# Performance work log

Measured on AMD Instinct MI355X. Metric: run time of the kernel, lower is better.

## Reference

```python
import jax, jax.numpy as jnp
import numpy as np

NF, NA, NC = 100000, 400, 30   # flight, airport, carrier node counts
N = NF + NA + NC               # total nodes after type concatenation
D = 256                        # hidden_channels
B = 3                          # num_bases
R = 4                          # num_relations
E = 250000                     # edges per relation


def setup_inputs() -> dict:
    key = jax.random.key(0)
    ks = jax.random.split(key, 32)
    inp = {
        'x_flight': jax.random.normal(ks[0], (NF, 32), jnp.float32),
        'x_airport': jax.random.normal(ks[1], (NA, 16), jnp.float32),
        'x_carrier': jax.random.normal(ks[2], (NC, 8), jnp.float32),
        # per-type encoders (Linear stored as [in, out])
        'W_f': jax.random.normal(ks[3], (32, D), jnp.float32) * 0.05,
        'b_f': jnp.zeros((D,), jnp.float32),
        'W_a': jax.random.normal(ks[4], (16, D), jnp.float32) * 0.05,
        'b_a': jnp.zeros((D,), jnp.float32),
        'W_c': jax.random.normal(ks[5], (8, D), jnp.float32) * 0.05,
        'b_c': jnp.zeros((D,), jnp.float32),
        # RGCNConv layer 0: basis decomposition W_r = sum_b comp[r,b] * basis[b]
        'basis0': jax.random.normal(ks[6], (B, D, D), jnp.float32) * 0.02,
        'comp0': jax.random.normal(ks[7], (R, B), jnp.float32) * 0.5,
        'root0': jax.random.normal(ks[8], (D, D), jnp.float32) * 0.02,
        'bias0': jnp.zeros((D,), jnp.float32),
        # RGCNConv layer 1
        'basis1': jax.random.normal(ks[9], (B, D, D), jnp.float32) * 0.02,
        'comp1': jax.random.normal(ks[10], (R, B), jnp.float32) * 0.5,
        'root1': jax.random.normal(ks[11], (D, D), jnp.float32) * 0.02,
        'bias1': jnp.zeros((D,), jnp.float32),
        # readout Linear(D -> 1)
        'W_out': jax.random.normal(ks[12], (D, 1), jnp.float32) * 0.05,
        'b_out': jnp.zeros((1,), jnp.float32),
        # per-relation edge lists (local indices within src/dst node type)
        'src0': jax.random.randint(ks[13], (E,), 0, NF),
        'dst0': jax.random.randint(ks[14], (E,), 0, NA),
        'src1': jax.random.randint(ks[15], (E,), 0, NA),
        'dst1': jax.random.randint(ks[16], (E,), 0, NF),
        'src2': jax.random.randint(ks[17], (E,), 0, NF),
        'dst2': jax.random.randint(ks[18], (E,), 0, NC),
        'src3': jax.random.randint(ks[19], (E,), 0, NC),
        'dst3': jax.random.randint(ks[20], (E,), 0, NF),
    }
    return inp


def _rgcn_conv(x, basis, comp, root, bias, edges):
    """PyG RGCNConv with basis decomposition, mean aggregation per relation."""
    W = jnp.einsum('rb,bio->rio', comp, basis)  # [R, D, D]
    out = x @ root + bias                        # root/self transform
    for r, (src, dst) in enumerate(edges):       # R=4 fixed relations
        msg = x[src] @ W[r]                                        # [E, D]
        agg = jax.ops.segment_sum(msg, dst, num_segments=N)        # [N, D]
        deg = jax.ops.segment_sum(jnp.ones((dst.shape[0],), x.dtype), dst,
                                  num_segments=N)
        out = out + agg / jnp.maximum(deg, 1.0)[:, None]           # mean aggr
    return out


def reference(x_flight, x_airport, x_carrier,
              W_f, b_f, W_a, b_a, W_c, b_c,
              basis0, comp0, root0, bias0,
              basis1, comp1, root1, bias1,
              W_out, b_out,
              src0, dst0, src1, dst1, src2, dst2, src3, dst3):
    # per-type encoders + ReLU, then concat into homogeneous node tensor
    hf = jax.nn.relu(x_flight @ W_f + b_f)
    ha = jax.nn.relu(x_airport @ W_a + b_a)
    hc = jax.nn.relu(x_carrier @ W_c + b_c)
    x = jnp.concatenate([hf, ha, hc], axis=0)  # offsets: flight=0, airport=NF, carrier=NF+NA
    edges = [
        (src0, dst0 + NF),        # flight -> airport
        (src1 + NF, dst1),        # airport -> flight
        (src2, dst2 + NF + NA),   # flight -> carrier
        (src3 + NF + NA, dst3),   # carrier -> flight
    ]
    x = jax.nn.relu(_rgcn_conv(x, basis0, comp0, root0, bias0, edges))
    x = jax.nn.relu(_rgcn_conv(x, basis1, comp1, root1, bias1, edges))
    # dropout is identity in eval mode
    return (x[:NF] @ W_out + b_out).squeeze(-1)  # [NF]
```

## Files before the change

### kernel.cpp

```cpp
#include <hip/hip_runtime.h>
#include <hip/hip_bf16.h>
#include <cstdint>
#include <cstddef>

constexpr int NF = 100000;
constexpr int NA = 400;
constexpr int NC = 30;
constexpr int NN = NF + NA + NC;
constexpr int D  = 256;
constexpr int DD = D * D;
constexpr int E  = 250000;
constexpr int NSL = 128;
constexpr int FBLK = (NF + 127) / 128;
constexpr int TAILB = (NA + NC + 7) / 8;
constexpr int F13B = (2 * E + 511) / 512;
constexpr int AGGB = NA * 4 + NC * 64;
constexpr int YB   = (NA + NC) / 2;

constexpr int K1_HIST_END = 2 * NSL;
constexpr int K1_DEG_END  = K1_HIST_END + (2 * E + 255) / 256;
constexpr int K1_WS0_END  = K1_DEG_END + 256;
constexpr int K1_WS1_END  = K1_WS0_END + 256;
constexpr int K1_WR0_END  = K1_WS1_END + 1024;
constexpr int K1_WR1_END  = K1_WR0_END + 1024;

constexpr int W_ENC_END  = FBLK;
constexpr int W_TAIL_END = W_ENC_END + TAILB;
constexpr int W_F13_END  = W_TAIL_END + F13B;
constexpr int W_TOTAL    = W_F13_END + 2 * NSL;

typedef __attribute__((ext_vector_type(8))) short bf16x8;
typedef __attribute__((ext_vector_type(4))) float f32x4;
typedef __attribute__((ext_vector_type(8))) ushort u16x8;

__device__ inline ushort f2bf(float f) {
    __hip_bfloat16 h = __float2bfloat16(f);
    return __builtin_bit_cast(ushort, h);
}
__device__ inline float bf2f(ushort u) {
    __hip_bfloat16 h = __builtin_bit_cast(__hip_bfloat16, u);
    return __bfloat162float(h);
}

__device__ inline void gload_lds16(const ushort* g, ushort* l) {
    __builtin_amdgcn_global_load_lds(
        (const __attribute__((address_space(1))) void*)g,
        (__attribute__((address_space(3))) void*)l, 16, 0, 0);
}

__global__ __launch_bounds__(256) void prep_kernel(
    const int* __restrict__ dst0, const int* __restrict__ dst2,
    int* __restrict__ bh0, int* __restrict__ bh2,
    float* __restrict__ aggz,
    const float* __restrict__ Wf, ushort* __restrict__ WfTH, ushort* __restrict__ WfTL,
    const int* __restrict__ dst1, const int* __restrict__ dst3,
    int* __restrict__ deg1, int* __restrict__ deg3,
    const float* __restrict__ root0, ushort* __restrict__ WtH0, ushort* __restrict__ WtL0,
    const float* __restrict__ root1, ushort* __restrict__ WtH1, ushort* __restrict__ WtL1,
    const float* __restrict__ basis0, const float* __restrict__ comp0, float* __restrict__ wr0,
    const float* __restrict__ basis1, const float* __restrict__ comp1, float* __restrict__ wr1)
{
    __shared__ int hist[NA];
    const int b = blockIdx.x;
    const int t = threadIdx.x;
    if (b < K1_HIST_END) {
        for (int i = b * 256 + t; i < (NA + NC) * D; i += K1_HIST_END * 256)
            aggz[i] = 0.f;
        if (b < 32) {
            float wv = Wf[(size_t)b * D + t];
            ushort hi = f2bf(wv);
            WfTH[(size_t)t * 32 + b] = hi;
            WfTL[(size_t)t * 32 + b] = f2bf(wv - bf2f(hi));
        }
        bool isR2 = (b >= NSL);
        int sl = isR2 ? b - NSL : b;
        const int* dst = isR2 ? dst2 : dst0;
        int nb = isR2 ? NC : NA;
        for (int i = t; i < nb; i += 256) hist[i] = 0;
        __syncthreads();
        int lo = (int)((long long)E * sl / NSL);
        int hi = (int)((long long)E * (sl + 1) / NSL);
        for (int e = lo + t; e < hi; e += 256)
            atomicAdd(&hist[dst[e]], 1);
        __syncthreads();
        int* bh = isR2 ? (bh2 + sl * NC) : (bh0 + sl * NA);
        for (int i = t; i < nb; i += 256) bh[i] = hist[i];
    } else if (b < K1_DEG_END) {
        int idx = (b - K1_HIST_END) * 256 + t;
        if (idx < 2 * E) {
            if (idx < E) atomicAdd(&deg1[dst1[idx]], 1);
            else         atomicAdd(&deg3[dst3[idx - E]], 1);
        }
    } else if (b < K1_WS0_END) {
        int n = b - K1_DEG_END;
        float w = root0[(size_t)t * D + n];
        ushort hi = f2bf(w);
        WtH0[(size_t)n * D + t] = hi;
        WtL0[(size_t)n * D + t] = f2bf(w - bf2f(hi));
    } else if (b < K1_WS1_END) {
        int n = b - K1_WS0_END;
        float w = root1[(size_t)t * D + n];
        ushort hi = f2bf(w);
        WtH1[(size_t)n * D + t] = hi;
        WtL1[(size_t)n * D + t] = f2bf(w - bf2f(hi));
    } else if (b < K1_WR0_END) {
        int idx = (b - K1_WS1_END) * 256 + t;
        int r = idx >> 16;
        int io = idx & (DD - 1);
        wr0[idx] = comp0[r * 3 + 0] * basis0[io]
                 + comp0[r * 3 + 1] * basis0[DD + io]
                 + comp0[r * 3 + 2] * basis0[2 * DD + io];
    } else {
        int idx = (b - K1_WR0_END) * 256 + t;
        int r = idx >> 16;
        int io = idx & (DD - 1);
        wr1[idx] = comp1[r * 3 + 0] * basis1[io]
                 + comp1[r * 3 + 1] * basis1[DD + io]
                 + comp1[r * 3 + 2] * basis1[2 * DD + io];
    }
}

__global__ __launch_bounds__(1024) void scan_kernel(
    const int* __restrict__ deg1, const int* __restrict__ deg3,
    int* __restrict__ bsum,
    int* __restrict__ bh0, int* __restrict__ bh2,
    int* __restrict__ rp0, int* __restrict__ rp2,
    float* __restrict__ inv0, float* __restrict__ inv2)
{
    __shared__ int s[1024];
    __shared__ int tot[512];
    __shared__ int exc[512];
    const int b = blockIdx.x;
    const int t = threadIdx.x;
    if (b < 196) {
        bool isR3 = (b >= 98);
        const int* deg = isR3 ? deg3 : deg1;
        int chunk = isR3 ? b - 98 : b;
        int i = chunk * 1024 + t;
        int v = (i < NF) ? deg[i] : 0;
        s[t] = v;
        __syncthreads();
        for (int ofs = 512; ofs > 0; ofs >>= 1) {
            if (t < ofs) s[t] += s[t + ofs];
            __syncthreads();
        }
        if (t == 0) bsum[(isR3 ? 128 : 0) + chunk] = s[0];
        return;
    }
    int cnt = 0;
    if (t < NA) {
        int ss = 0;
        for (int sl = 0; sl < NSL; ++sl) {
            int v = bh0[sl * NA + t]; bh0[sl * NA + t] = ss; ss += v;
        }
        cnt = ss;
    } else if (t < NA + NC) {
        int bin = t - NA; int ss = 0;
        for (int sl = 0; sl < NSL; ++sl) {
            int v = bh2[sl * NC + bin]; bh2[sl * NC + bin] = ss; ss += v;
        }
        cnt = ss;
    }
    if (t < 512) tot[t] = cnt;
    __syncthreads();
    for (int ofs = 1; ofs < 512; ofs <<= 1) {
        int v = 0;
        if (t < 512 && t >= ofs) v = tot[t - ofs];
        __syncthreads();
        if (t < 512) tot[t] += v;
        __syncthreads();
    }
    if (t < 512) {
        int ex = tot[t] - cnt;
        if (t < NA) {
            exc[t] = ex;
            rp0[t] = ex;
            inv0[t] = 1.0f / (float)(cnt > 1 ? cnt : 1);
            if (t == 0) { rp0[NA] = E; rp2[NC] = E; }
        } else if (t < NA + NC) {
            exc[t] = ex - E;
            rp2[t - NA] = ex - E;
            inv2[t - NA] = 1.0f / (float)(cnt > 1 ? cnt : 1);
        } else exc[t] = 0;
    }
    __syncthreads();
    for (int idx = t; idx < NSL * NA; idx += 1024) {
        int sl = idx / NA; int bin = idx - sl * NA;
        bh0[idx] += exc[bin];
    }
    for (int idx = t; idx < NSL * NC; idx += 1024) {
        int sl = idx / NC; int bin = idx - sl * NC;
        bh2[idx] += exc[NA + bin];
    }
}

__global__ __launch_bounds__(1024) void scanC_kernel(
    const int* __restrict__ deg1, const int* __restrict__ deg3,
    const int* __restrict__ bsum,
    int* __restrict__ rp1, int* __restrict__ rp3,
    int* __restrict__ cu1, int* __restrict__ cu3,
    float* __restrict__ inv1, float* __restrict__ inv3)
{
    __shared__ int s[1024];
    __shared__ int s2[256];
    int t = threadIdx.x;
    int b = blockIdx.x;
    int vb = 0;
    if (t < 256) {
        vb = ((t & 127) < 98) ? bsum[t] : 0;
        s2[t] = vb;
    }
    __syncthreads();
    for (int ofs = 1; ofs < 128; ofs <<= 1) {
        int a = 0;
        if (t < 256 && (t & 127) >= ofs) a = s2[t - ofs];
        __syncthreads();
        if (t < 256) s2[t] += a;
        __syncthreads();
    }
    if (t < 256) s2[t] -= vb;
    __syncthreads();
    const int* deg; int* rp; int* cu; float* inv; int chunk; int prefix;
    if (b < 98) { deg = deg1; rp = rp1; cu = cu1; inv = inv1; chunk = b;      prefix = s2[chunk]; }
    else        { deg = deg3; rp = rp3; cu = cu3; inv = inv3; chunk = b - 98; prefix = s2[128 + chunk]; }
    int i = chunk * 1024 + t;
    int v = (i < NF) ? deg[i] : 0;
    s[t] = v;
    __syncthreads();
    for (int ofs = 1; ofs < 1024; ofs <<= 1) {
        int a = (t >= ofs) ? s[t - ofs] : 0;
        __syncthreads();
        s[t] += a;
        __syncthreads();
    }
    int ex = prefix + s[t] - v;
    if (i < NF) {
        rp[i] = ex;
        cu[i] = ex;
        inv[i] = 1.0f / (float)(v > 1 ? v : 1);
    }
    if (i == 0) rp[NF] = E;
}

__global__ __launch_bounds__(512) void work_kernel(
    const float* __restrict__ xf,
    const ushort* __restrict__ WtH8, const ushort* __restrict__ WtL8,
    const float* __restrict__ bfl,
    const float* __restrict__ xa, const float* __restrict__ Wa, const float* __restrict__ ba,
    const float* __restrict__ xc, const float* __restrict__ Wc, const float* __restrict__ bc,
    ushort* __restrict__ hH,
    const int* __restrict__ src1, const int* __restrict__ dst1,
    const int* __restrict__ src3, const int* __restrict__ dst3,
    int* __restrict__ cu1, int* __restrict__ cu3,
    int* __restrict__ csr1, int* __restrict__ csr3,
    const int* __restrict__ src0, const int* __restrict__ dst0,
    const int* __restrict__ src2, const int* __restrict__ dst2,
    const int* __restrict__ bh0, const int* __restrict__ bh2,
    int* __restrict__ csr0, int* __restrict__ csr2)
{
    __shared__ __align__(16) ushort lds[20480];
    const int t = threadIdx.x;
    const int b = blockIdx.x;
    if (b >= W_F13_END) {
        int bb = b - W_F13_END;
        int* cur = (int*)lds;
        bool isR2 = (bb >= NSL);
        int sl = isR2 ? bb - NSL : bb;
        const int* src = isR2 ? src2 : src0;
        const int* dst = isR2 ? dst2 : dst0;
        const int* bh  = isR2 ? (bh2 + sl * NC) : (bh0 + sl * NA);
        int* csr       = isR2 ? csr2 : csr0;
        int nb = isR2 ? NC : NA;
        for (int i = t; i < nb; i += 512) cur[i] = bh[i];
        __syncthreads();
        int lo = (int)((long long)E * sl / NSL);
        int hi = (int)((long long)E * (sl + 1) / NSL);
        for (int e = lo + t; e < hi; e += 512) {
            int pos = atomicAdd(&cur[dst[e]], 1);
            csr[pos] = src[e];
        }
        return;
    }
    if (b >= W_TAIL_END) {
        int idx = (b - W_TAIL_END) * 512 + t;
        if (idx < 2 * E) {
            if (idx < E) {
                int pos = atomicAdd(&cu1[dst1[idx]], 1);
                csr1[pos] = src1[idx];
            } else {
                int e = idx - E;
                int pos = atomicAdd(&cu3[dst3[e]], 1);
                csr3[pos] = src3[e];
            }
        }
        return;
    }
    if (b >= W_ENC_END) {
        int c = t & 255;
        int i0 = t >> 8;
        int base = (b - W_ENC_END) * 8;
        for (int i = i0; i < 8; i += 2) {
            int row = base + i;
            if (row >= NA + NC) break;
            float acc;
            if (row < NA) {
                const float* xr = xa + (size_t)row * 16;
                acc = ba[c];
                #pragma unroll
                for (int k = 0; k < 16; ++k) acc += xr[k] * Wa[k * D + c];
            } else {
                const float* xr = xc + (size_t)(row - NA) * 8;
                acc = bc[c];
                #pragma unroll
                for (int k = 0; k < 8; ++k) acc += xr[k] * Wc[k * D + c];
            }
            hH[(size_t)(NF + row) * D + c] = f2bf(fmaxf(acc, 0.f));
        }
        return;
    }
    constexpr int AOFF = 0, WHOFF = 4096, WLOFF = 12288;
    const int row0 = b * 128;
    const int w = t >> 6, lane = t & 63;
    const int wm = w >> 2, wn = w & 3;
    const int lr = lane & 15;
    const int lk = lane >> 4;
    {
        int r = t >> 2;
        int seg = (t & 3) * 8;
        int gr = row0 + r; if (gr >= NF) gr = NF - 1;
        const float* xr = xf + (size_t)gr * 32 + seg;
        float4 a0 = *(const float4*)xr;
        float4 a1 = *(const float4*)(xr + 4);
        u16x8 bb;
        bb[0] = f2bf(a0.x); bb[1] = f2bf(a0.y); bb[2] = f2bf(a0.z); bb[3] = f2bf(a0.w);
        bb[4] = f2bf(a1.x); bb[5] = f2bf(a1.y); bb[6] = f2bf(a1.z); bb[7] = f2bf(a1.w);
        int g = r >> 4, rr = r & 15, kg = seg >> 3;
        *(u16x8*)(lds + AOFF + g * 512 + (rr + 16 * kg) * 8) = bb;
    }
    #pragma unroll
    for (int i = 0; i < 4; ++i) {
        int u = w * 4 + i;
        int plane = u >> 4, g = u & 15;
        const ushort* src = (plane ? WtL8 : WtH8) + ((size_t)(g * 16 + lr)) * 32 + lk * 8;
        ushort* dst = lds + (plane ? WLOFF : WHOFF) + g * 512;
        gload_lds16(src, dst);
    }
    __syncthreads();
    f32x4 acc[4][4] = {};
    bf16x8 bhv[4], blv[4];
    #pragma unroll
    for (int ni = 0; ni < 4; ++ni) {
        int off = (wn * 4 + ni) * 512 + lane * 8;
        bhv[ni] = *(const bf16x8*)(lds + WHOFF + off);
        blv[ni] = *(const bf16x8*)(lds + WLOFF + off);
    }
    #pragma unroll
    for (int mi = 0; mi < 4; ++mi) {
        bf16x8 ah = *(const bf16x8*)(lds + AOFF + (wm * 4 + mi) * 512 + lane * 8);
        #pragma unroll
        for (int ni = 0; ni < 4; ++ni) {
            acc[mi][ni] = __builtin_amdgcn_mfma_f32_16x16x32_bf16(ah, bhv[ni], acc[mi][ni], 0, 0, 0);
            acc[mi][ni] = __builtin_amdgcn_mfma_f32_16x16x32_bf16(ah, blv[ni], acc[mi][ni], 0, 0, 0);
        }
    }
    constexpr int ELDW = 68;
    float* S = (float*)lds + (size_t)w * 16 * ELDW;
    const int rrow = lane >> 3;
    const int grp  = lane & 7;
    #pragma unroll
    for (int mi = 0; mi < 4; ++mi) {
        __syncthreads();
        #pragma unroll
        for (int ni = 0; ni < 4; ++ni)
            #pragma unroll
            for (int reg = 0; reg < 4; ++reg)
                S[(lk * 4 + reg) * ELDW + ni * 16 + lr] = acc[mi][ni][reg];
        __syncthreads();
        #pragma unroll
        for (int it = 0; it < 2; ++it) {
            int row_i = rrow + it * 8;
            int gr = row0 + wm * 64 + mi * 16 + row_i;
            int gc = wn * 64 + grp * 8;
            if (gr >= NF) continue;
            float4 f0 = *(const float4*)(&S[row_i * ELDW + grp * 8]);
            float4 f1 = *(const float4*)(&S[row_i * ELDW + grp * 8 + 4]);
            float4 b0 = *(const float4*)(bfl + gc);
            float4 b1 = *(const float4*)(bfl + gc + 4);
            u16x8 hh;
            hh[0] = f2bf(fmaxf(f0.x + b0.x, 0.f));
            hh[1] = f2bf(fmaxf(f0.y + b0.y, 0.f));
            hh[2] = f2bf(fmaxf(f0.z + b0.z, 0.f));
            hh[3] = f2bf(fmaxf(f0.w + b0.w, 0.f));
            hh[4] = f2bf(fmaxf(f1.x + b1.x, 0.f));
            hh[5] = f2bf(fmaxf(f1.y + b1.y, 0.f));
            hh[6] = f2bf(fmaxf(f1.z + b1.z, 0.f));
            hh[7] = f2bf(fmaxf(f1.w + b1.w, 0.f));
            *(u16x8*)(hH + (size_t)gr * D + gc) = hh;
        }
    }
}

template<int MODE>
__global__ __launch_bounds__(512) void layer_kernel(
    const ushort* __restrict__ A,
    const ushort* __restrict__ WtH, const ushort* __restrict__ WtL,
    const float* __restrict__ bias, ushort* __restrict__ G,
    const float* __restrict__ wr, float* __restrict__ y,
    const int* __restrict__ rp0, const int* __restrict__ csr0,
    const int* __restrict__ rp2, const int* __restrict__ csr2,
    float* __restrict__ agg)
{
    constexpr int BM = 128, BK = 32;
    constexpr int PLANE = BM * BK;
    constexpr int BUF = 3 * PLANE;
    constexpr int LDW = 36;
    constexpr int nrows = (MODE == 0) ? NN : NF;
    constexpr int NT = (nrows + 127) / 128;
    constexpr int NG = NT * 2;
    constexpr int G8 = (NT / 8) * 16;
    constexpr int NAGG = (MODE == 0) ? AGGB : 0;
    __shared__ __align__(16) ushort lds[2 * BUF];
    const int t = threadIdx.x;
    const int b = blockIdx.x;
    if (b >= NG) {
        int bb = b - NG;
        if (MODE == 0 && bb < NAGG) {
            float* red = (float*)lds;
            const int* rp; const int* csr; int dstn, chunk, nch; float* arow;
            if (bb < NA * 4) { dstn = bb >> 2; chunk = bb & 3; nch = 4;  rp = rp0; csr = csr0; arow = agg + (size_t)dstn * D; }
            else { int b2 = bb - NA * 4; dstn = b2 >> 6; chunk = b2 & 63; nch = 64; rp = rp2; csr = csr2; arow = agg + (size_t)(NA + dstn) * D; }
            int s = rp[dstn], e = rp[dstn + 1];
            int cnt = e - s;
            int lo = s + (int)((long long)cnt * chunk / nch);
            int hi = s + (int)((long long)cnt * (chunk + 1) / nch);
            int w8 = t >> 6, lane = t & 63;
            int span = hi - lo;
            int wlo = lo + (int)((long long)span * w8 / 8);
            int whi = lo + (int)((long long)span * (w8 + 1) / 8);
            int half = lane >> 5;
            int ch8 = (lane & 31) * 8;
            float acc[8] = {};
            int p = wlo;
            for (; p + 1 < whi; p += 2) {
                int r = csr[p + half];
                u16x8 v = *(const u16x8*)(A + (size_t)r * D + ch8);
                #pragma unroll
                for (int j = 0; j < 8; ++j) acc[j] += bf2f(v[j]);
            }
            if (p < whi && half == 0) {
                int r = csr[p];
                u16x8 v = *(const u16x8*)(A + (size_t)r * D + ch8);
                #pragma unroll
                for (int j = 0; j < 8; ++j) acc[j] += bf2f(v[j]);
            }
            #pragma unroll
            for (int j = 0; j < 8; ++j) acc[j] += __shfl_xor(acc[j], 32);
            if (lane < 32) {
                #pragma unroll
                for (int j = 0; j < 8; ++j) red[w8 * 256 + ch8 + j] = acc[j];
            }
            __syncthreads();
            if (t < 256) {
                float total = 0.f;
                #pragma unroll
                for (int j = 0; j < 8; ++j) total += red[j * 256 + t];
                atomicAdd(arow + t, total);
            }
            return;
        }
        int yb = bb - NAGG;
        int row = yb * 2 + (t >> 8);
        if (row < NA + NC) {
            int c = t & 255;
            const ushort* sH = A + (size_t)(NF + row) * D;
            const float* W = wr + (size_t)((row < NA) ? 1 : 3) * DD;
            float acc = 0.f;
            #pragma unroll 8
            for (int k = 0; k < D; ++k) acc += bf2f(sH[k]) * W[k * D + c];
            y[(size_t)row * D + c] = acc;
        }
        return;
    }
    int rtile, ctile;
    if (b < G8) {
        int g = b >> 4, j = b & 15;
        rtile = g * 8 + (j & 7);
        ctile = j >> 3;
    } else {
        int j = b - G8;
        rtile = (NT / 8) * 8 + (j >> 1);
        ctile = j & 1;
    }
    const int row0 = rtile * BM;
    const int col0 = ctile * BM;
    const int w = t >> 6, lane = t & 63;
    const int wm = w >> 2, wn = w & 3;
    const int lr = lane & 15;
    const int lk = lane >> 4;
    f32x4 acc[4][2] = {};

    const ushort* sp[3];
    int dofs[3];
    #pragma unroll
    for (int i = 0; i < 3; ++i) {
        int idx = w * 3 + i;
        int plane = idx >> 3, g = idx & 7;
        const ushort* base = (plane == 0) ? A : (plane == 1) ? WtH : WtL;
        int r = ((plane == 0) ? row0 : col0) + g * 16 + lr;
        if (plane == 0 && r >= nrows) r = nrows - 1;
        sp[i] = base + (size_t)r * D + lk * 8;
        dofs[i] = plane * PLANE + g * 512;
    }

    auto stage = [&](int kt, int buf) {
        ushort* bb2 = lds + buf * BUF;
        int k0 = kt * BK;
        #pragma unroll
        for (int i = 0; i < 3; ++i)
            gload_lds16(sp[i] + k0, bb2 + dofs[i]);
    };
    auto compute = [&](int buf) {
        const ushort* base = lds + buf * BUF;
        const ushort* As  = base;
        const ushort* WsH = base + PLANE;
        const ushort* WsL = base + 2 * PLANE;
        bf16x8 bh[2], bl[2];
        #pragma unroll
        for (int ni = 0; ni < 2; ++ni) {
            int off = (wn * 2 + ni) * 512 + lane * 8;
            bh[ni] = *(const bf16x8*)(&WsH[off]);
            bl[ni] = *(const bf16x8*)(&WsL[off]);
        }
        #pragma unroll
        for (int mi = 0; mi < 4; ++mi) {
            int off = (wm * 4 + mi) * 512 + lane * 8;
            bf16x8 ah = *(const bf16x8*)(&As[off]);
            #pragma unroll
            for (int ni = 0; ni < 2; ++ni) {
                acc[mi][ni] = __builtin_amdgcn_mfma_f32_16x16x32_bf16(ah, bh[ni], acc[mi][ni], 0, 0, 0);
                acc[mi][ni] = __builtin_amdgcn_mfma_f32_16x16x32_bf16(ah, bl[ni], acc[mi][ni], 0, 0, 0);
            }
        }
    };

    stage(0, 0);
    stage(1, 1);
#define PIPE_ITER(KT, PEND)                                        \
    asm volatile("s_waitcnt vmcnt(" #PEND ")" ::: "memory");       \
    __builtin_amdgcn_s_barrier();                                  \
    __builtin_amdgcn_sched_barrier(0);                             \
    compute((KT) & 1);                                             \
    __builtin_amdgcn_s_barrier();                                  \
    __builtin_amdgcn_sched_barrier(0);                             \
    if ((KT) + 2 < 8) stage((KT) + 2, (KT) & 1);
    PIPE_ITER(0, 3)
    PIPE_ITER(1, 3)
    PIPE_ITER(2, 3)
    PIPE_ITER(3, 3)
    PIPE_ITER(4, 3)
    PIPE_ITER(5, 3)
    PIPE_ITER(6, 3)
    PIPE_ITER(7, 0)
#undef PIPE_ITER

    __syncthreads();
    float* S = (float*)lds + (size_t)w * 16 * LDW;
    const int rrow = lane >> 2;
    const int grp  = lane & 3;
    #pragma unroll
    for (int mi = 0; mi < 4; ++mi) {
        __syncthreads();
        #pragma unroll
        for (int ni = 0; ni < 2; ++ni)
            #pragma unroll
            for (int reg = 0; reg < 4; ++reg)
                S[(lk * 4 + reg) * LDW + ni * 16 + lr] = acc[mi][ni][reg];
        __syncthreads();
        int gr = row0 + wm * 64 + mi * 16 + rrow;
        int gc = col0 + wn * 32 + grp * 8;
        if (gr >= nrows) continue;
        float4 f0 = *(const float4*)(&S[rrow * LDW + grp * 8]);
        float4 f1 = *(const float4*)(&S[rrow * LDW + grp * 8 + 4]);
        float4 b0 = *(const float4*)(bias + gc);
        float4 b1 = *(const float4*)(bias + gc + 4);
        float v[8] = {f0.x + b0.x, f0.y + b0.y, f0.z + b0.z, f0.w + b0.w,
                      f1.x + b1.x, f1.y + b1.y, f1.z + b1.z, f1.w + b1.w};
        u16x8 hh;
        #pragma unroll
        for (int j = 0; j < 8; ++j) hh[j] = f2bf(v[j]);
        *(u16x8*)(G + (size_t)gr * D + gc) = hh;
    }
}

__global__ __launch_bounds__(256) void finish0_kernel(
    const float* __restrict__ agg, const float* __restrict__ wr,
    const float* __restrict__ inv0, const float* __restrict__ inv2,
    ushort* __restrict__ G,
    const float* __restrict__ y,
    const int* __restrict__ rp1, const int* __restrict__ csr1, const float* __restrict__ inv1,
    const int* __restrict__ rp3, const int* __restrict__ csr3, const float* __restrict__ inv3)
{
    const int b = blockIdx.x;
    const int t = threadIdx.x;
    if (b < NA + NC) {
        int row = b;
        int c = t;
        const float* a = agg + (size_t)row * D;
        const float* W = wr + (size_t)((row < NA) ? 0 : 2) * DD;
        float scale = (row < NA) ? inv0[row] : inv2[row - NA];
        float acc = 0.f;
        #pragma unroll 8
        for (int k = 0; k < D; ++k) acc += a[k] * W[k * D + c];
        size_t o = (size_t)(NF + row) * D + c;
        G[o] = f2bf(fmaxf(bf2f(G[o]) + scale * acc, 0.f));
        return;
    }
    int wid = ((b - (NA + NC)) * 256 + t) >> 6;
    int lane = t & 63;
    int row = wid * 2 + (lane >> 5);
    if (row >= NF) return;
    int c = (lane & 31) * 8;
    size_t o = (size_t)row * D + c;
    u16x8 gh = *(const u16x8*)(G + o);
    float v[8];
    #pragma unroll
    for (int j = 0; j < 8; ++j) v[j] = bf2f(gh[j]);
    float m[8] = {};
    int e0 = rp1[row], e1 = rp1[row + 1];
    for (int e = e0; e < e1; ++e) {
        const float* yr = y + (size_t)csr1[e] * D + c;
        float4 u0 = *(const float4*)yr;
        float4 u1 = *(const float4*)(yr + 4);
        m[0] += u0.x; m[1] += u0.y; m[2] += u0.z; m[3] += u0.w;
        m[4] += u1.x; m[5] += u1.y; m[6] += u1.z; m[7] += u1.w;
    }
    float s1 = inv1[row];
    #pragma unroll
    for (int j = 0; j < 8; ++j) { v[j] += s1 * m[j]; m[j] = 0.f; }
    e0 = rp3[row]; e1 = rp3[row + 1];
    for (int e = e0; e < e1; ++e) {
        const float* yr = y + (size_t)(NA + csr3[e]) * D + c;
        float4 u0 = *(const float4*)yr;
        float4 u1 = *(const float4*)(yr + 4);
        m[0] += u0.x; m[1] += u0.y; m[2] += u0.z; m[3] += u0.w;
        m[4] += u1.x; m[5] += u1.y; m[6] += u1.z; m[7] += u1.w;
    }
    float s3 = inv3[row];
    u16x8 oh;
    #pragma unroll
    for (int j = 0; j < 8; ++j) oh[j] = f2bf(fmaxf(v[j] + s3 * m[j], 0.f));
    *(u16x8*)(G + o) = oh;
}

__global__ __launch_bounds__(256) void msg_readout_kernel(
    const ushort* __restrict__ G,
    const float* __restrict__ y,
    const int* __restrict__ rp1, const int* __restrict__ csr1, const float* __restrict__ inv1,
    const int* __restrict__ rp3, const int* __restrict__ csr3, const float* __restrict__ inv3,
    const float* __restrict__ wout, const float* __restrict__ bout,
    float* __restrict__ out)
{
    int wid = (blockIdx.x * 256 + threadIdx.x) >> 6;
    int lane = threadIdx.x & 63;
    int row = wid * 2 + (lane >> 5);
    if (row >= NF) return;
    int c = (lane & 31) * 8;
    size_t o = (size_t)row * D + c;
    u16x8 gh = *(const u16x8*)(G + o);
    float v[8];
    #pragma unroll
    for (int j = 0; j < 8; ++j) v[j] = bf2f(gh[j]);
    float m[8] = {};
    int e0 = rp1[row], e1 = rp1[row + 1];
    for (int e = e0; e < e1; ++e) {
        const float* yr = y + (size_t)csr1[e] * D + c;
        float4 u0 = *(const float4*)yr;
        float4 u1 = *(const float4*)(yr + 4);
        m[0] += u0.x; m[1] += u0.y; m[2] += u0.z; m[3] += u0.w;
        m[4] += u1.x; m[5] += u1.y; m[6] += u1.z; m[7] += u1.w;
    }
    float s1 = inv1[row];
    #pragma unroll
    for (int j = 0; j < 8; ++j) { v[j] += s1 * m[j]; m[j] = 0.f; }
    e0 = rp3[row]; e1 = rp3[row + 1];
    for (int e = e0; e < e1; ++e) {
        const float* yr = y + (size_t)(NA + csr3[e]) * D + c;
        float4 u0 = *(const float4*)yr;
        float4 u1 = *(const float4*)(yr + 4);
        m[0] += u0.x; m[1] += u0.y; m[2] += u0.z; m[3] += u0.w;
        m[4] += u1.x; m[5] += u1.y; m[6] += u1.z; m[7] += u1.w;
    }
    float s3 = inv3[row];
    float4 w0 = *(const float4*)(wout + c);
    float4 w1 = *(const float4*)(wout + c + 4);
    float wv[8] = {w0.x, w0.y, w0.z, w0.w, w1.x, w1.y, w1.z, w1.w};
    float pr = 0.f;
    #pragma unroll
    for (int j = 0; j < 8; ++j) pr += fmaxf(v[j] + s3 * m[j], 0.f) * wv[j];
    pr += __shfl_xor(pr, 1);
    pr += __shfl_xor(pr, 2);
    pr += __shfl_xor(pr, 4);
    pr += __shfl_xor(pr, 8);
    pr += __shfl_xor(pr, 16);
    if ((lane & 31) == 0) out[row] = pr + bout[0];
}

extern "C" void kernel_launch(void* const* d_in, const int* in_sizes, int n_in,
                              void* d_out, int out_size, void* d_ws, size_t ws_size,
                              hipStream_t stream)
{
    const float* xf = (const float*)d_in[0];
    const float* xa = (const float*)d_in[1];
    const float* xc = (const float*)d_in[2];
    const float* Wf = (const float*)d_in[3];
    const float* bf = (const float*)d_in[4];
    const float* Wa = (const float*)d_in[5];
    const float* ba = (const float*)d_in[6];
    const float* Wc = (const float*)d_in[7];
    const float* bc = (const float*)d_in[8];
    const float* basis0 = (const float*)d_in[9];
    const float* comp0  = (const float*)d_in[10];
    const float* root0  = (const float*)d_in[11];
    const float* bias0  = (const float*)d_in[12];
    const float* basis1 = (const float*)d_in[13];
    const float* comp1  = (const float*)d_in[14];
    const float* root1  = (const float*)d_in[15];
    const float* bias1  = (const float*)d_in[16];
    const float* Wout = (const float*)d_in[17];
    const float* bout = (const float*)d_in[18];
    const int* src0 = (const int*)d_in[19];
    const int* dst0 = (const int*)d_in[20];
    const int* src1 = (const int*)d_in[21];
    const int* dst1 = (const int*)d_in[22];
    const int* src2 = (const int*)d_in[23];
    const int* dst2 = (const int*)d_in[24];
    const int* src3 = (const int*)d_in[25];
    const int* dst3 = (const int*)d_in[26];
    float* out = (float*)d_out;

    char* ws = (char*)d_ws;
    size_t off = 0;
    auto alloc = [&](size_t bytes) -> char* {
        char* p = ws + off;
        off = (off + bytes + 255) & ~(size_t)255;
        return p;
    };
    ushort* hH  = (ushort*)alloc((size_t)NN * D * 2);
    ushort* gH  = (ushort*)alloc((size_t)NN * D * 2);
    ushort* g2H = hH;
    ushort* WtH0 = (ushort*)alloc((size_t)DD * 2);
    ushort* WtL0 = (ushort*)alloc((size_t)DD * 2);
    ushort* WtH1 = (ushort*)alloc((size_t)DD * 2);
    ushort* WtL1 = (ushort*)alloc((size_t)DD * 2);
    ushort* WfTH = (ushort*)alloc((size_t)D * 32 * 2);
    ushort* WfTL = (ushort*)alloc((size_t)D * 32 * 2);
    float* wr0    = (float*)alloc((size_t)4 * DD * 4);
    float* wr1    = (float*)alloc((size_t)4 * DD * 4);
    float* ybuf   = (float*)alloc((size_t)(NA + NC) * D * 4);
    float* aggbuf = (float*)alloc((size_t)(NA + NC) * D * 4);
    int*   deg13  = (int*)  alloc((size_t)2 * NF * 4);
    int* deg1 = deg13; int* deg3 = deg13 + NF;
    float* inv1 = (float*)alloc((size_t)NF * 4);
    float* inv3 = (float*)alloc((size_t)NF * 4);
    float* inv0 = (float*)alloc((size_t)NA * 4);
    float* inv2 = (float*)alloc((size_t)NC * 4);
    int* rp0 = (int*)alloc((NA + 1) * 4);
    int* rp1 = (int*)alloc((size_t)(NF + 1) * 4);
    int* rp2 = (int*)alloc((NC + 1) * 4);
    int* rp3 = (int*)alloc((size_t)(NF + 1) * 4);
    int* cu1 = (int*)alloc((size_t)(NF + 1) * 4);
    int* cu3 = (int*)alloc((size_t)(NF + 1) * 4);
    int* csr0 = (int*)alloc((size_t)E * 4);
    int* csr1 = (int*)alloc((size_t)E * 4);
    int* csr2 = (int*)alloc((size_t)E * 4);
    int* csr3 = (int*)alloc((size_t)E * 4);
    int* bsum = (int*)alloc(256 * 4);
    int* bh0  = (int*)alloc((size_t)NSL * NA * 4);
    int* bh2  = (int*)alloc((size_t)NSL * NC * 4);
    (void)ws_size; (void)in_sizes; (void)n_in; (void)out_size;

    hipMemsetAsync(deg13, 0, (size_t)2 * NF * 4, stream);

    prep_kernel<<<K1_WR1_END, 256, 0, stream>>>(
        dst0, dst2, bh0, bh2, aggbuf, Wf, WfTH, WfTL,
        dst1, dst3, deg1, deg3,
        root0, WtH0, WtL0, root1, WtH1, WtL1,
        basis0, comp0, wr0, basis1, comp1, wr1);

    scan_kernel<<<197, 1024, 0, stream>>>(
        deg1, deg3, bsum, bh0, bh2, rp0, rp2, inv0, inv2);

    scanC_kernel<<<196, 1024, 0, stream>>>(
        deg1, deg3, bsum, rp1, rp3, cu1, cu3, inv1, inv3);

    work_kernel<<<W_TOTAL, 512, 0, stream>>>(
        xf, WfTH, WfTL, bf, xa, Wa, ba, xc, Wc, bc, hH,
        src1, dst1, src3, dst3, cu1, cu3, csr1, csr3,
        src0, dst0, src2, dst2, bh0, bh2, csr0, csr2);

    constexpr int NG0 = ((NN + 127) / 128) * 2;
    layer_kernel<0><<<NG0 + AGGB + YB, 512, 0, stream>>>(
        hH, WtH0, WtL0, bias0, gH, wr0, ybuf,
        rp0, csr0, rp2, csr2, aggbuf);
    finish0_kernel<<<(NA + NC) + (NF / 2 * 64 + 255) / 256, 256, 0, stream>>>(
        aggbuf, wr0, inv0, inv2, gH,
        ybuf, rp1, csr1, inv1, rp3, csr3, inv3);

    constexpr int NG1 = ((NF + 127) / 128) * 2;
    layer_kernel<1><<<NG1 + YB, 512, 0, stream>>>(
        gH, WtH1, WtL1, bias1, g2H, wr1, ybuf,
        nullptr, nullptr, nullptr, nullptr, nullptr);
    msg_readout_kernel<<<(NF / 2 * 64 + 255) / 256, 256, 0, stream>>>(
        g2H, ybuf, rp1, csr1, inv1, rp3, csr3, inv3, Wout, bout, out);
}
```

Baseline: 325.5 us.

## Fuse message gathers into GEMM epilogues and readout into layer-1 kernel

The airport/carrier source-side projections y = h·W_r now move earlier: layer-0 projections go into the encoder tail blocks and layer-1 projections into finish0. This lets each layer's GEMM epilogue gather the flight-destination messages directly. The layer-1 epilogue also performs the readout dot product with atomicAdd into an output pre-set to the bias. This drops two standalone gather kernels and a full round-trip of the 100k×256 node tensor, at the cost of heavier, irregular epilogues inside the GEMM tiles and float atomics on the output.

```diff
diff --git a/kernel.cpp b/kernel.cpp
--- a/kernel.cpp
+++ b/kernel.cpp
@@ -15,7 +15,6 @@
 constexpr int TAILB = (NA + NC + 7) / 8;
 constexpr int F13B = (2 * E + 511) / 512;
 constexpr int AGGB = NA * 4 + NC * 64;
-constexpr int YB   = (NA + NC) / 2;
 
 constexpr int K1_HIST_END = 2 * NSL;
 constexpr int K1_DEG_END  = K1_HIST_END + (2 * E + 255) / 256;
@@ -256,7 +255,8 @@
     const int* __restrict__ src0, const int* __restrict__ dst0,
     const int* __restrict__ src2, const int* __restrict__ dst2,
     const int* __restrict__ bh0, const int* __restrict__ bh2,
-    int* __restrict__ csr0, int* __restrict__ csr2)
+    int* __restrict__ csr0, int* __restrict__ csr2,
+    const float* __restrict__ wr0, float* __restrict__ y0)
 {
     __shared__ __align__(16) ushort lds[20480];
     const int t = threadIdx.x;
@@ -296,25 +296,42 @@
         return;
     }
     if (b >= W_ENC_END) {
+        float* hrow = (float*)lds;
         int c = t & 255;
         int i0 = t >> 8;
         int base = (b - W_ENC_END) * 8;
         for (int i = i0; i < 8; i += 2) {
             int row = base + i;
+            float val = 0.f;
+            if (row < NA + NC) {
+                float acc;
+                if (row < NA) {
+                    const float* xr = xa + (size_t)row * 16;
+                    acc = ba[c];
+                    #pragma unroll
+                    for (int k = 0; k < 16; ++k) acc += xr[k] * Wa[k * D + c];
+                } else {
+                    const float* xr = xc + (size_t)(row - NA) * 8;
+                    acc = bc[c];
+                    #pragma unroll
+                    for (int k = 0; k < 8; ++k) acc += xr[k] * Wc[k * D + c];
+                }
+                ushort hv = f2bf(fmaxf(acc, 0.f));
+                hH[(size_t)(NF + row) * D + c] = hv;
+                val = bf2f(hv);
+            }
+            hrow[i * 256 + c] = val;
+        }
+        __syncthreads();
+        for (int i = i0; i < 8; i += 2) {
+            int row = base + i;
             if (row >= NA + NC) break;
-            float acc;
-            if (row < NA) {
-                const float* xr = xa + (size_t)row * 16;
-                acc = ba[c];
-                #pragma unroll
-                for (int k = 0; k < 16; ++k) acc += xr[k] * Wa[k * D + c];
-            } else {
-                const float* xr = xc + (size_t)(row - NA) * 8;
-                acc = bc[c];
-                #pragma unroll
-                for (int k = 0; k < 8; ++k) acc += xr[k] * Wc[k * D + c];
-            }
-            hH[(size_t)(NF + row) * D + c] = f2bf(fmaxf(acc, 0.f));
+            const float* W = wr0 + (size_t)((row < NA) ? 1 : 3) * DD;
+            const float* hr = hrow + i * 256;
+            float acc = 0.f;
+            #pragma unroll 8
+            for (int k = 0; k < D; ++k) acc += hr[k] * W[k * D + c];
+            y0[(size_t)row * D + c] = acc;
         }
         return;
     }
@@ -405,10 +422,13 @@
     const ushort* __restrict__ A,
     const ushort* __restrict__ WtH, const ushort* __restrict__ WtL,
     const float* __restrict__ bias, ushort* __restrict__ G,
-    const float* __restrict__ wr, float* __restrict__ y,
     const int* __restrict__ rp0, const int* __restrict__ csr0,
     const int* __restrict__ rp2, const int* __restrict__ csr2,
-    float* __restrict__ agg)
+    float* __restrict__ agg,
+    const float* __restrict__ ybuf,
+    const int* __restrict__ rp1, const int* __restrict__ csr1, const float* __restrict__ inv1,
+    const int* __restrict__ rp3, const int* __restrict__ csr3, const float* __restrict__ inv3,
+    const float* __restrict__ wout, float* __restrict__ outp)
 {
     constexpr int BM = 128, BK = 32;
     constexpr int PLANE = BM * BK;
@@ -418,66 +438,51 @@
     constexpr int NT = (nrows + 127) / 128;
     constexpr int NG = NT * 2;
     constexpr int G8 = (NT / 8) * 16;
-    constexpr int NAGG = (MODE == 0) ? AGGB : 0;
     __shared__ __align__(16) ushort lds[2 * BUF];
     const int t = threadIdx.x;
     const int b = blockIdx.x;
-    if (b >= NG) {
+    if (MODE == 0 && b >= NG) {
         int bb = b - NG;
-        if (MODE == 0 && bb < NAGG) {
-            float* red = (float*)lds;
-            const int* rp; const int* csr; int dstn, chunk, nch; float* arow;
-            if (bb < NA * 4) { dstn = bb >> 2; chunk = bb & 3; nch = 4;  rp = rp0; csr = csr0; arow = agg + (size_t)dstn * D; }
-            else { int b2 = bb - NA * 4; dstn = b2 >> 6; chunk = b2 & 63; nch = 64; rp = rp2; csr = csr2; arow = agg + (size_t)(NA + dstn) * D; }
-            int s = rp[dstn], e = rp[dstn + 1];
-            int cnt = e - s;
-            int lo = s + (int)((long long)cnt * chunk / nch);
-            int hi = s + (int)((long long)cnt * (chunk + 1) / nch);
-            int w8 = t >> 6, lane = t & 63;
-            int span = hi - lo;
-            int wlo = lo + (int)((long long)span * w8 / 8);
-            int whi = lo + (int)((long long)span * (w8 + 1) / 8);
-            int half = lane >> 5;
-            int ch8 = (lane & 31) * 8;
-            float acc[8] = {};
-            int p = wlo;
-            for (; p + 1 < whi; p += 2) {
-                int r = csr[p + half];
-                u16x8 v = *(const u16x8*)(A + (size_t)r * D + ch8);
-                #pragma unroll
-                for (int j = 0; j < 8; ++j) acc[j] += bf2f(v[j]);
-            }
-            if (p < whi && half == 0) {
-                int r = csr[p];
-                u16x8 v = *(const u16x8*)(A + (size_t)r * D + ch8);
-                #pragma unroll
-                for (int j = 0; j < 8; ++j) acc[j] += bf2f(v[j]);
-            }
-            #pragma unroll
-            for (int j = 0; j < 8; ++j) acc[j] += __shfl_xor(acc[j], 32);
-            if (lane < 32) {
-                #pragma unroll
-                for (int j = 0; j < 8; ++j) red[w8 * 256 + ch8 + j] = acc[j];
-            }
-            __syncthreads();
-            if (t < 256) {
-                float total = 0.f;
-                #pragma unroll
-                for (int j = 0; j < 8; ++j) total += red[j * 256 + t];
-                atomicAdd(arow + t, total);
-            }
-            return;
-        }
-        int yb = bb - NAGG;
-        int row = yb * 2 + (t >> 8);
-        if (row < NA + NC) {
-            int c = t & 255;
-            const ushort* sH = A + (size_t)(NF + row) * D;
-            const float* W = wr + (size_t)((row < NA) ? 1 : 3) * DD;
-            float acc = 0.f;
-            #pragma unroll 8
-            for (int k = 0; k < D; ++k) acc += bf2f(sH[k]) * W[k * D + c];
-            y[(size_t)row * D + c] = acc;
+        float* red = (float*)lds;
+        const int* rp; const int* csr; int dstn, chunk, nch; float* arow;
+        if (bb < NA * 4) { dstn = bb >> 2; chunk = bb & 3; nch = 4;  rp = rp0; csr = csr0; arow = agg + (size_t)dstn * D; }
+        else { int b2 = bb - NA * 4; dstn = b2 >> 6; chunk = b2 & 63; nch = 64; rp = rp2; csr = csr2; arow = agg + (size_t)(NA + dstn) * D; }
+        int s = rp[dstn], e = rp[dstn + 1];
+        int cnt = e - s;
+        int lo = s + (int)((long long)cnt * chunk / nch);
+        int hi = s + (int)((long long)cnt * (chunk + 1) / nch);
+        int w8 = t >> 6, lane = t & 63;
+        int span = hi - lo;
+        int wlo = lo + (int)((long long)span * w8 / 8);
+        int whi = lo + (int)((long long)span * (w8 + 1) / 8);
+        int half = lane >> 5;
+        int ch8 = (lane & 31) * 8;
+        float acc[8] = {};
+        int p = wlo;
+        for (; p + 1 < whi; p += 2) {
+            int r = csr[p + half];
+            u16x8 v = *(const u16x8*)(A + (size_t)r * D + ch8);
+            #pragma unroll
+            for (int j = 0; j < 8; ++j) acc[j] += bf2f(v[j]);
+        }
+        if (p < whi && half == 0) {
+            int r = csr[p];
+            u16x8 v = *(const u16x8*)(A + (size_t)r * D + ch8);
+            #pragma unroll
+            for (int j = 0; j < 8; ++j) acc[j] += bf2f(v[j]);
+        }
+        #pragma unroll
+        for (int j = 0; j < 8; ++j) acc[j] += __shfl_xor(acc[j], 32);
+        if (lane < 32) {
+            #pragma unroll
+            for (int j = 0; j < 8; ++j) red[w8 * 256 + ch8 + j] = acc[j];
+        }
+        __syncthreads();
+        if (t < 256) {
+            float total = 0.f;
+            #pragma unroll
+            for (int j = 0; j < 8; ++j) total += red[j * 256 + t];
+            atomicAdd(arow + t, total);
         }
         return;
     }
@@ -585,124 +590,104 @@
         float4 b1 = *(const float4*)(bias + gc + 4);
         float v[8] = {f0.x + b0.x, f0.y + b0.y, f0.z + b0.z, f0.w + b0.w,
                       f1.x + b1.x, f1.y + b1.y, f1.z + b1.z, f1.w + b1.w};
-        u16x8 hh;
-        #pragma unroll
-        for (int j = 0; j < 8; ++j) hh[j] = f2bf(v[j]);
-        *(u16x8*)(G + (size_t)gr * D + gc) = hh;
+        if (MODE == 0) {
+            if (gr < NF) {
+                float m[8] = {};
+                int e0 = rp1[gr], e1 = rp1[gr + 1];
+                for (int e = e0; e < e1; ++e) {
+                    const float* yr = ybuf + (size_t)csr1[e] * D + gc;
+                    float4 u0 = *(const float4*)yr;
+                    float4 u1 = *(const float4*)(yr + 4);
+                    m[0] += u0.x; m[1] += u0.y; m[2] += u0.z; m[3] += u0.w;
+                    m[4] += u1.x; m[5] += u1.y; m[6] += u1.z; m[7] += u1.w;
+                }
+                float s1 = inv1[gr];
+                #pragma unroll
+                for (int j = 0; j < 8; ++j) { v[j] += s1 * m[j]; m[j] = 0.f; }
+                e0 = rp3[gr]; e1 = rp3[gr + 1];
+                for (int e = e0; e < e1; ++e) {
+                    const float* yr = ybuf + (size_t)(NA + csr3[e]) * D + gc;
+                    float4 u0 = *(const float4*)yr;
+                    float4 u1 = *(const float4*)(yr + 4);
+                    m[0] += u0.x; m[1] += u0.y; m[2] += u0.z; m[3] += u0.w;
+                    m[4] += u1.x; m[5] += u1.y; m[6] += u1.z; m[7] += u1.w;
+                }
+                float s3 = inv3[gr];
+                #pragma unroll
+                for (int j = 0; j < 8; ++j) v[j] = fmaxf(v[j] + s3 * m[j], 0.f);
+            }
+            u16x8 hh;
+            #pragma unroll
+            for (int j = 0; j < 8; ++j) hh[j] = f2bf(v[j]);
+            *(u16x8*)(G + (size_t)gr * D + gc) = hh;
+        } else {
+            float m[8] = {};
+            int e0 = rp1[gr], e1 = rp1[gr + 1];
+            for (int e = e0; e < e1; ++e) {
+                const float* yr = ybuf + (size_t)csr1[e] * D + gc;
+                float4 u0 = *(const float4*)yr;
+                float4 u1 = *(const float4*)(yr + 4);
+                m[0] += u0.x; m[1] += u0.y; m[2] += u0.z; m[3] += u0.w;
+                m[4] += u1.x; m[5] += u1.y; m[6] += u1.z; m[7] += u1.w;
+            }
+            float s1 = inv1[gr];
+            #pragma unroll
+            for (int j = 0; j < 8; ++j) { v[j] += s1 * m[j]; m[j] = 0.f; }
+            e0 = rp3[gr]; e1 = rp3[gr + 1];
+            for (int e = e0; e < e1; ++e) {
+                const float* yr = ybuf + (size_t)(NA + csr3[e]) * D + gc;
+                float4 u0 = *(const float4*)yr;
+                float4 u1 = *(const float4*)(yr + 4);
+                m[0] += u0.x; m[1] += u0.y; m[2] += u0.z; m[3] += u0.w;
+                m[4] += u1.x; m[5] += u1.y; m[6] += u1.z; m[7] += u1.w;
+            }
+            float s3 = inv3[gr];
+            float4 w0 = *(const float4*)(wout + gc);
+            float4 w1 = *(const float4*)(wout + gc + 4);
+            float wv[8] = {w0.x, w0.y, w0.z, w0.w, w1.x, w1.y, w1.z, w1.w};
+            float pr = 0.f;
+            #pragma unroll
+            for (int j = 0; j < 8; ++j) pr += fmaxf(v[j] + s3 * m[j], 0.f) * wv[j];
+            pr += __shfl_xor(pr, 1);
+            pr += __shfl_xor(pr, 2);
+            if (grp == 0) atomicAdd(outp + gr, pr);
+        }
     }
 }
 
 __global__ __launch_bounds__(256) void finish0_kernel(
-    const float* __restrict__ agg, const float* __restrict__ wr,
+    const float* __restrict__ agg, const float* __restrict__ wr0,
+    const float* __restrict__ wr1,
     const float* __restrict__ inv0, const float* __restrict__ inv2,
-    ushort* __restrict__ G,
-    const float* __restrict__ y,
-    const int* __restrict__ rp1, const int* __restrict__ csr1, const float* __restrict__ inv1,
-    const int* __restrict__ rp3, const int* __restrict__ csr3, const float* __restrict__ inv3)
+    ushort* __restrict__ G, float* __restrict__ y1,
+    float* __restrict__ outp, const float* __restrict__ bout)
 {
+    __shared__ float grow[256];
     const int b = blockIdx.x;
     const int t = threadIdx.x;
     if (b < NA + NC) {
         int row = b;
         int c = t;
         const float* a = agg + (size_t)row * D;
-        const float* W = wr + (size_t)((row < NA) ? 0 : 2) * DD;
+        const float* W = wr0 + (size_t)((row < NA) ? 0 : 2) * DD;
         float scale = (row < NA) ? inv0[row] : inv2[row - NA];
         float acc = 0.f;
         #pragma unroll 8
         for (int k = 0; k < D; ++k) acc += a[k] * W[k * D + c];
         size_t o = (size_t)(NF + row) * D + c;
-        G[o] = f2bf(fmaxf(bf2f(G[o]) + scale * acc, 0.f));
+        ushort hv = f2bf(fmaxf(bf2f(G[o]) + scale * acc, 0.f));
+        G[o] = hv;
+        grow[c] = bf2f(hv);
+        __syncthreads();
+        const float* W1 = wr1 + (size_t)((row < NA) ? 1 : 3) * DD;
+        float acc2 = 0.f;
+        #pragma unroll 8
+        for (int k = 0; k < D; ++k) acc2 += grow[k] * W1[k * D + c];
+        y1[(size_t)row * D + c] = acc2;
         return;
     }
-    int wid = ((b - (NA + NC)) * 256 + t) >> 6;
-    int lane = t & 63;
-    int row = wid * 2 + (lane >> 5);
-    if (row >= NF) return;
-    int c = (lane & 31) * 8;
-    size_t o = (size_t)row * D + c;
-    u16x8 gh = *(const u16x8*)(G + o);
-    float v[8];
-    #pragma unroll
-    for (int j = 0; j < 8; ++j) v[j] = bf2f(gh[j]);
-    float m[8] = {};
-    int e0 = rp1[row], e1 = rp1[row + 1];
-    for (int e = e0; e < e1; ++e) {
-        const float* yr = y + (size_t)csr1[e] * D + c;
-        float4 u0 = *(const float4*)yr;
-        float4 u1 = *(const float4*)(yr + 4);
-        m[0] += u0.x; m[1] += u0.y; m[2] += u0.z; m[3] += u0.w;
-        m[4] += u1.x; m[5] += u1.y; m[6] += u1.z; m[7] += u1.w;
-    }
-    float s1 = inv1[row];
-    #pragma unroll
-    for (int j = 0; j < 8; ++j) { v[j] += s1 * m[j]; m[j] = 0.f; }
-    e0 = rp3[row]; e1 = rp3[row + 1];
-    for (int e = e0; e < e1; ++e) {
-        const float* yr = y + (size_t)(NA + csr3[e]) * D + c;
-        float4 u0 = *(const float4*)yr;
-        float4 u1 = *(const float4*)(yr + 4);
-        m[0] += u0.x; m[1] += u0.y; m[2] += u0.z; m[3] += u0.w;
-        m[4] += u1.x; m[5] += u1.y; m[6] += u1.z; m[7] += u1.w;
-    }
-    float s3 = inv3[row];
-    u16x8 oh;
-    #pragma unroll
-    for (int j = 0; j < 8; ++j) oh[j] = f2bf(fmaxf(v[j] + s3 * m[j], 0.f));
-    *(u16x8*)(G + o) = oh;
-}
-
-__global__ __launch_bounds__(256) void msg_readout_kernel(
-    const ushort* __restrict__ G,
-    const float* __restrict__ y,
-    const int* __restrict__ rp1, const int* __restrict__ csr1, const float* __restrict__ inv1,
-    const int* __restrict__ rp3, const int* __restrict__ csr3, const float* __restrict__ inv3,
-    const float* __restrict__ wout, const float* __restrict__ bout,
-    float* __restrict__ out)
-{
-    int wid = (blockIdx.x * 256 + threadIdx.x) >> 6;
-    int lane = threadIdx.x & 63;
-    int row = wid * 2 + (lane >> 5);
-    if (row >= NF) return;
-    int c = (lane & 31) * 8;
-    size_t o = (size_t)row * D + c;
-    u16x8 gh = *(const u16x8*)(G + o);
-    float v[8];
-    #pragma unroll
-    for (int j = 0; j < 8; ++j) v[j] = bf2f(gh[j]);
-    float m[8] = {};
-    int e0 = rp1[row], e1 = rp1[row + 1];
-    for (int e = e0; e < e1; ++e) {
-        const float* yr = y + (size_t)csr1[e] * D + c;
-        float4 u0 = *(const float4*)yr;
-        float4 u1 = *(const float4*)(yr + 4);
-        m[0] += u0.x; m[1] += u0.y; m[2] += u0.z; m[3] += u0.w;
-        m[4] += u1.x; m[5] += u1.y; m[6] += u1.z; m[7] += u1.w;
-    }
-    float s1 = inv1[row];
-    #pragma unroll
-    for (int j = 0; j < 8; ++j) { v[j] += s1 * m[j]; m[j] = 0.f; }
-    e0 = rp3[row]; e1 = rp3[row + 1];
-    for (int e = e0; e < e1; ++e) {
-        const float* yr = y + (size_t)(NA + csr3[e]) * D + c;
-        float4 u0 = *(const float4*)yr;
-        float4 u1 = *(const float4*)(yr + 4);
-        m[0] += u0.x; m[1] += u0.y; m[2] += u0.z; m[3] += u0.w;
-        m[4] += u1.x; m[5] += u1.y; m[6] += u1.z; m[7] += u1.w;
-    }
-    float s3 = inv3[row];
-    float4 w0 = *(const float4*)(wout + c);
-    float4 w1 = *(const float4*)(wout + c + 4);
-    float wv[8] = {w0.x, w0.y, w0.z, w0.w, w1.x, w1.y, w1.z, w1.w};
-    float pr = 0.f;
-    #pragma unroll
-    for (int j = 0; j < 8; ++j) pr += fmaxf(v[j] + s3 * m[j], 0.f) * wv[j];
-    pr += __shfl_xor(pr, 1);
-    pr += __shfl_xor(pr, 2);
-    pr += __shfl_xor(pr, 4);
-    pr += __shfl_xor(pr, 8);
-    pr += __shfl_xor(pr, 16);
-    if ((lane & 31) == 0) out[row] = pr + bout[0];
+    int idx = (b - (NA + NC)) * 256 + t;
+    if (idx < NF) outp[idx] = bout[0];
 }
 
 extern "C" void kernel_launch(void* const* d_in, const int* in_sizes, int n_in,
@@ -747,7 +732,6 @@
     };
     ushort* hH  = (ushort*)alloc((size_t)NN * D * 2);
     ushort* gH  = (ushort*)alloc((size_t)NN * D * 2);
-    ushort* g2H = hH;
     ushort* WtH0 = (ushort*)alloc((size_t)DD * 2);
     ushort* WtL0 = (ushort*)alloc((size_t)DD * 2);
     ushort* WtH1 = (ushort*)alloc((size_t)DD * 2);
@@ -796,20 +780,24 @@
     work_kernel<<<W_TOTAL, 512, 0, stream>>>(
         xf, WfTH, WfTL, bf, xa, Wa, ba, xc, Wc, bc, hH,
         src1, dst1, src3, dst3, cu1, cu3, csr1, csr3,
-        src0, dst0, src2, dst2, bh0, bh2, csr0, csr2);
+        src0, dst0, src2, dst2, bh0, bh2, csr0, csr2,
+        wr0, ybuf);
 
     constexpr int NG0 = ((NN + 127) / 128) * 2;
-    layer_kernel<0><<<NG0 + AGGB + YB, 512, 0, stream>>>(
-        hH, WtH0, WtL0, bias0, gH, wr0, ybuf,
-        rp0, csr0, rp2, csr2, aggbuf);
-    finish0_kernel<<<(NA + NC) + (NF / 2 * 64 + 255) / 256, 256, 0, stream>>>(
-        aggbuf, wr0, inv0, inv2, gH,
-        ybuf, rp1, csr1, inv1, rp3, csr3, inv3);
+    layer_kernel<0><<<NG0 + AGGB, 512, 0, stream>>>(
+        hH, WtH0, WtL0, bias0, gH,
+        rp0, csr0, rp2, csr2, aggbuf,
+        ybuf, rp1, csr1, inv1, rp3, csr3, inv3,
+        nullptr, nullptr);
+
+    constexpr int OUTB = (NF + 255) / 256;
+    finish0_kernel<<<(NA + NC) + OUTB, 256, 0, stream>>>(
+        aggbuf, wr0, wr1, inv0, inv2, gH, ybuf, out, bout);
 
     constexpr int NG1 = ((NF + 127) / 128) * 2;
-    layer_kernel<1><<<NG1 + YB, 512, 0, stream>>>(
-        gH, WtH1, WtL1, bias1, g2H, wr1, ybuf,
-        nullptr, nullptr, nullptr, nullptr, nullptr);
-    msg_readout_kernel<<<(NF / 2 * 64 + 255) / 256, 256, 0, stream>>>(
-        g2H, ybuf, rp1, csr1, inv1, rp3, csr3, inv3, Wout, bout, out);
-}
+    layer_kernel<1><<<NG1, 512, 0, stream>>>(
+        gH, WtH1, WtL1, bias1, nullptr,
+        nullptr, nullptr, nullptr, nullptr, nullptr,
+        ybuf, rp1, csr1, inv1, rp3, csr3, inv3,
+        Wout, out);
+}
```

After: 388.8 us. +19.5%, slower.
